# Optimization experiments

Measured on AMD Instinct MI355X. Metric: run time of the kernel, lower is better.

Reference implementation:

```python
import jax, jax.numpy as jnp
import numpy as np

TWO_PI = 2.0 * np.pi
MIN_W = 1e-3  # min bin width (nsf defaults)
MIN_H = 1e-3  # min bin height
MIN_D = 1e-3  # min derivative
NUM_BINS = 32
DERIV_OFFSET = float(np.log(np.e - 1.0))  # so softplus(x+offset)=1 at x=0


def setup_inputs() -> dict:
    key = jax.random.key(0)
    k0, k1, k2, k3 = jax.random.split(key, 4)
    B, N, H, nb, d = 1048576, 64, 256, NUM_BINS, 1
    theta = jax.random.uniform(k0, (B, d), dtype=jnp.float32) * TWO_PI
    x_conditioner = jax.random.normal(k1, (B, N), dtype=jnp.float32)
    W1 = jax.random.normal(k2, (N, H), dtype=jnp.float32) / np.sqrt(N)
    b1 = jnp.zeros((H,), jnp.float32)
    W2 = jax.random.normal(k3, (H, 3 * nb * d), dtype=jnp.float32) / np.sqrt(H)
    b2 = jnp.zeros((3 * nb * d,), jnp.float32)
    eta = jnp.ones((1,), jnp.float32)  # rezero_flag=False -> fixed 1
    return {"theta": theta, "x_conditioner": x_conditioner,
            "W1": W1, "b1": b1, "W2": W2, "b2": b2, "eta": eta}


def _make_knots(unnorm, min_size, left, right):
    # normalized bin sizes -> cumulative knot positions on [left, right]
    nb = unnorm.shape[-1]
    sizes = MIN_W * 0 + min_size + (1.0 - min_size * nb) * jax.nn.softmax(unnorm, axis=-1)
    cum = jnp.cumsum(sizes, axis=-1)
    cum = jnp.concatenate([jnp.zeros_like(cum[..., :1]), cum], axis=-1)
    cum = (right - left) * cum + left
    cum = cum.at[..., 0].set(left)
    cum = cum.at[..., -1].set(right)
    sizes = cum[..., 1:] - cum[..., :-1]
    return cum, sizes


def _circular_rq_spline(inputs, uw, uh, ud, left=0.0, right=TWO_PI):
    # inputs: (B, d); uw/uh/ud: (B, d, nb)
    nb = uw.shape[-1]
    cumwidths, widths = _make_knots(uw, MIN_W, left, right)
    cumheights, heights = _make_knots(uh, MIN_H, left, right)  # circular: bottom=left, top=right
    # circular boundary: derivative at last knot == derivative at first knot
    ud_p = jnp.concatenate([ud, ud[..., :1]], axis=-1)  # (B, d, nb+1)
    derivatives = MIN_D + jax.nn.softplus(ud_p)

    # bin search (searchsorted equivalent)
    bin_idx = jnp.clip(jnp.sum(inputs[..., None] >= cumwidths, axis=-1) - 1, 0, nb - 1)  # (B, d)
    idx = bin_idx[..., None]
    g = lambda t: jnp.take_along_axis(t, idx, axis=-1)[..., 0]

    in_cw = g(cumwidths)
    in_w = g(widths)
    in_ch = g(cumheights)
    in_h = g(heights)
    d_k = g(derivatives)
    d_k1 = jnp.take_along_axis(derivatives, idx + 1, axis=-1)[..., 0]
    delta = in_h / in_w  # bin slope s_k

    th = (inputs - in_cw) / in_w
    th_om = th * (1.0 - th)
    denominator = delta + (d_k1 + d_k - 2.0 * delta) * th_om
    numerator = in_h * (delta * th * th + d_k * th_om)
    outputs = in_ch + numerator / denominator
    deriv_num = delta * delta * (d_k1 * th * th + 2.0 * delta * th_om + d_k * (1.0 - th) ** 2)
    logabsdet = jnp.log(deriv_num) - 2.0 * jnp.log(denominator)
    return outputs, logabsdet


def reference(theta, x_conditioner, W1, b1, W2, b2, eta):
    B, d = theta.shape
    nb = NUM_BINS
    h = jax.nn.relu(x_conditioner @ W1 + b1)
    params = (h @ W2 + b2) * eta
    params = params.reshape(B, d, 3 * nb)
    uw, uh, ud = jnp.split(params, 3, axis=-1)
    ud = ud + DERIV_OFFSET
    theta_out, logabsdet = _circular_rq_spline(theta, uw, uh, ud)
    return theta_out, logabsdet
```

## Files before the change

kernel.cpp:

```cpp
#include <hip/hip_runtime.h>


typedef _Float16 f16x8 __attribute__((ext_vector_type(8)));
typedef float    f32x4 __attribute__((ext_vector_type(4)));

#define TWO_PI_F  6.28318530717958647692f
#define MIN_SZ    1e-3f
#define MIN_D_F   1e-3f
#define DERIV_OFF 0.54132485461291810f

__device__ __forceinline__ float softplus_f(float x) {
    return fmaxf(x, 0.f) + log1pf(__expf(-fabsf(x)));
}

__global__ void flow_prep(const float* __restrict__ W1, const float* __restrict__ W2,
                          _Float16* __restrict__ w1h, _Float16* __restrict__ w1l,
                          _Float16* __restrict__ w2h, _Float16* __restrict__ w2l) {
    int i = blockIdx.x * 256 + threadIdx.x;
    if (i < 16384) {
        int j = i & 7, l = (i >> 3) & 63, kx = (i >> 9) & 1, ht = i >> 10;
        int h = ht * 16 + (l & 15);
        int k = kx * 32 + (l >> 4) * 8 + j;
        float v = W1[k * 256 + h];
        _Float16 hv = (_Float16)v;
        w1h[i] = hv;
        w1l[i] = (_Float16)(v - (float)hv);
    }
    int i2 = i - 16384;
    if (i2 >= 0 && i2 < 24576) {
        int j = i2 & 7, l = (i2 >> 3) & 63, kb = (i2 >> 9) & 7, pt = i2 >> 12;
        int p = pt * 16 + (l & 15);
        int h = (2 * kb + (j >> 2)) * 16 + ((l >> 4) << 2) + (j & 3);
        float v = W2[h * 96 + p];
        _Float16 hv = (_Float16)v;
        w2h[i2] = hv;
        w2l[i2] = (_Float16)(v - (float)hv);
    }
}

__global__ __launch_bounds__(256, 3) void flow_main(
    const float* __restrict__ theta, const float* __restrict__ xc,
    const float* __restrict__ b1g, const float* __restrict__ b2g,
    const float* __restrict__ etag,
    const _Float16* __restrict__ w1h, const _Float16* __restrict__ w1l,
    const _Float16* __restrict__ w2h, const _Float16* __restrict__ w2l,
    float* __restrict__ out, int Btot)
{
    __shared__ __align__(16) float sP[4 * 32 * 97];
    __shared__ float sB1[256];
    __shared__ float sB2[96];

    const int t   = threadIdx.x;
    const int wid = t >> 6;
    const int l   = t & 63;
    const int q   = l >> 4;
    const int lc  = l & 15;
    const long R0w = ((long)blockIdx.x * 4 + wid) * 32;

    if (t < 256) sB1[t] = b1g[t];
    if (t < 96)  sB2[t] = b2g[t];
    __syncthreads();
    const float ev = etag[0];

    float thA = 0.f;
    if (l < 32) thA = theta[R0w + l];

    const f16x8* w1vh = (const f16x8*)w1h;
    const f16x8* w1vl = (const f16x8*)w1l;
    const f16x8* w2vh = (const f16x8*)w2h;
    const f16x8* w2vl = (const f16x8*)w2l;

    f16x8 xh[2][2], xl[2][2];
    #pragma unroll
    for (int mt = 0; mt < 2; ++mt)
        #pragma unroll
        for (int kx = 0; kx < 2; ++kx) {
            const float* xp = xc + (R0w + mt * 16 + lc) * 64 + kx * 32 + q * 8;
            float4 v0 = *(const float4*)xp;
            float4 v1 = *(const float4*)(xp + 4);
            f16x8 hi, lo;
            hi[0] = (_Float16)v0.x; lo[0] = (_Float16)(v0.x - (float)hi[0]);
            hi[1] = (_Float16)v0.y; lo[1] = (_Float16)(v0.y - (float)hi[1]);
            hi[2] = (_Float16)v0.z; lo[2] = (_Float16)(v0.z - (float)hi[2]);
            hi[3] = (_Float16)v0.w; lo[3] = (_Float16)(v0.w - (float)hi[3]);
            hi[4] = (_Float16)v1.x; lo[4] = (_Float16)(v1.x - (float)hi[4]);
            hi[5] = (_Float16)v1.y; lo[5] = (_Float16)(v1.y - (float)hi[5]);
            hi[6] = (_Float16)v1.z; lo[6] = (_Float16)(v1.z - (float)hi[6]);
            hi[7] = (_Float16)v1.w; lo[7] = (_Float16)(v1.w - (float)hi[7]);
            xh[mt][kx] = hi;
            xl[mt][kx] = lo;
        }

    f32x4 acc2[6][2] = {};
    #pragma unroll 2
    for (int kb = 0; kb < 8; ++kb) {
        f32x4 a1[2][2] = {};
        #pragma unroll
        for (int i = 0; i < 2; ++i) {
            const int ht = 2 * kb + i;
            #pragma unroll
            for (int kx = 0; kx < 2; ++kx) {
                f16x8 wh = w1vh[(ht * 2 + kx) * 64 + l];
                f16x8 wl = w1vl[(ht * 2 + kx) * 64 + l];
                #pragma unroll
                for (int mt = 0; mt < 2; ++mt) {
                    a1[i][mt] = __builtin_amdgcn_mfma_f32_16x16x32_f16(wl, xh[mt][kx], a1[i][mt], 0, 0, 0);
                    a1[i][mt] = __builtin_amdgcn_mfma_f32_16x16x32_f16(wh, xl[mt][kx], a1[i][mt], 0, 0, 0);
                    a1[i][mt] = __builtin_amdgcn_mfma_f32_16x16x32_f16(wh, xh[mt][kx], a1[i][mt], 0, 0, 0);
                }
            }
        }
        f16x8 bh[2], bl[2];
        float4 bb0 = *(const float4*)(sB1 + (2 * kb + 0) * 16 + q * 4);
        float4 bb1 = *(const float4*)(sB1 + (2 * kb + 1) * 16 + q * 4);
        #pragma unroll
        for (int mt = 0; mt < 2; ++mt) {
            f16x8 hi, lo;
            float v;
            v = fmaxf(a1[0][mt][0] + bb0.x, 0.f); hi[0] = (_Float16)v; lo[0] = (_Float16)(v - (float)hi[0]);
            v = fmaxf(a1[0][mt][1] + bb0.y, 0.f); hi[1] = (_Float16)v; lo[1] = (_Float16)(v - (float)hi[1]);
            v = fmaxf(a1[0][mt][2] + bb0.z, 0.f); hi[2] = (_Float16)v; lo[2] = (_Float16)(v - (float)hi[2]);
            v = fmaxf(a1[0][mt][3] + bb0.w, 0.f); hi[3] = (_Float16)v; lo[3] = (_Float16)(v - (float)hi[3]);
            v = fmaxf(a1[1][mt][0] + bb1.x, 0.f); hi[4] = (_Float16)v; lo[4] = (_Float16)(v - (float)hi[4]);
            v = fmaxf(a1[1][mt][1] + bb1.y, 0.f); hi[5] = (_Float16)v; lo[5] = (_Float16)(v - (float)hi[5]);
            v = fmaxf(a1[1][mt][2] + bb1.z, 0.f); hi[6] = (_Float16)v; lo[6] = (_Float16)(v - (float)hi[6]);
            v = fmaxf(a1[1][mt][3] + bb1.w, 0.f); hi[7] = (_Float16)v; lo[7] = (_Float16)(v - (float)hi[7]);
            bh[mt] = hi;
            bl[mt] = lo;
        }
        #pragma unroll
        for (int pt = 0; pt < 6; ++pt) {
            f16x8 wh = w2vh[(pt * 8 + kb) * 64 + l];
            f16x8 wl = w2vl[(pt * 8 + kb) * 64 + l];
            #pragma unroll
            for (int mt = 0; mt < 2; ++mt) {
                acc2[pt][mt] = __builtin_amdgcn_mfma_f32_16x16x32_f16(wl, bh[mt], acc2[pt][mt], 0, 0, 0);
                acc2[pt][mt] = __builtin_amdgcn_mfma_f32_16x16x32_f16(wh, bl[mt], acc2[pt][mt], 0, 0, 0);
                acc2[pt][mt] = __builtin_amdgcn_mfma_f32_16x16x32_f16(wh, bh[mt], acc2[pt][mt], 0, 0, 0);
            }
        }
    }

    float* sPw = sP + wid * (32 * 97);
    #pragma unroll
    for (int pt = 0; pt < 6; ++pt) {
        float4 bb = *(const float4*)(sB2 + pt * 16 + q * 4);
        #pragma unroll
        for (int mtl = 0; mtl < 2; ++mtl) {
            f32x4 v = acc2[pt][mtl];
            float* dst = sPw + (mtl * 16 + lc) * 97 + pt * 16 + q * 4;
            dst[0] = (v[0] + bb.x) * ev;
            dst[1] = (v[1] + bb.y) * ev;
            dst[2] = (v[2] + bb.z) * ev;
            dst[3] = (v[3] + bb.w) * ev;
        }
    }
    {
        int row = l & 31;
        float* rowp = sPw + row * 97 + ((l >> 5) << 5);
        float mx = rowp[0];
        #pragma unroll
        for (int j = 1; j < 32; ++j) mx = fmaxf(mx, rowp[j]);
        float S = 0.f;
        #pragma unroll
        for (int j = 0; j < 32; ++j) {
            float e = __expf(rowp[j] - mx);
            rowp[j] = e;
            S += e;
        }
        float scale = (1.0f - 32.0f * MIN_SZ) / S;
        float c = 0.f;
        #pragma unroll
        for (int j = 0; j < 32; ++j) {
            c += rowp[j];
            rowp[j] = TWO_PI_F * fmaf(scale, c, MIN_SZ * (float)(j + 1));
        }
        rowp[31] = TWO_PI_F;
    }
    if (l < 32) {
        const float* row = sPw + l * 97;
        long gr = R0w + l;
        float th_in = thA;
        int bin = 0;
        #pragma unroll
        for (int j = 0; j < 32; ++j) bin += (th_in >= row[j]) ? 1 : 0;
        bin = min(bin, 31);

        float cwk1 = row[bin];
        float cwk0 = (bin == 0) ? 0.f : row[bin - 1];
        float chk1 = row[32 + bin];
        float chk0 = (bin == 0) ? 0.f : row[32 + bin - 1];
        float in_w = cwk1 - cwk0;
        float in_h = chk1 - chk0;
        float d_k  = MIN_D_F + softplus_f(row[64 + bin] + DERIV_OFF);
        float d_k1 = MIN_D_F + softplus_f(row[64 + ((bin + 1) & 31)] + DERIV_OFF);

        float s   = in_h / in_w;
        float tt  = (th_in - cwk0) / in_w;
        float tom = tt * (1.f - tt);
        float denom = s + (d_k1 + d_k - 2.f * s) * tom;
        float numer = in_h * (s * tt * tt + d_k * tom);
        float outv  = chk0 + numer / denom;
        float omt   = 1.f - tt;
        float dnum  = s * s * (d_k1 * tt * tt + 2.f * s * tom + d_k * omt * omt);
        float lad   = __logf(dnum) - 2.f * __logf(denom);

        out[gr]               = outv;
        out[(long)Btot + gr]  = lad;
    }
}

extern "C" void kernel_launch(void* const* d_in, const int* in_sizes, int n_in,
                              void* d_out, int out_size, void* d_ws, size_t ws_size,
                              hipStream_t stream) {
    const float* theta = (const float*)d_in[0];
    const float* xcond = (const float*)d_in[1];
    const float* W1    = (const float*)d_in[2];
    const float* b1    = (const float*)d_in[3];
    const float* W2    = (const float*)d_in[4];
    const float* b2    = (const float*)d_in[5];
    const float* eta   = (const float*)d_in[6];
    int Btot = in_sizes[0];

    _Float16* w1h = (_Float16*)d_ws;
    _Float16* w1l = w1h + 16384;
    _Float16* w2h = w1l + 16384;
    _Float16* w2l = w2h + 24576;

    flow_prep<<<160, 256, 0, stream>>>(W1, W2, w1h, w1l, w2h, w2l);
    flow_main<<<Btot / 128, 256, 0, stream>>>(theta, xcond, b1, b2, eta,
                                              w1h, w1l, w2h, w2l,
                                              (float*)d_out, Btot);
}
```

Baseline: 556.7 us.

## Halve LDS staging by processing spline tail in two 16-row rounds

The epilogue now stages only 16 rows of spline parameters per wave in LDS and processes the two M-tiles in sequence. This halves shared memory per block and raises the launch-bounds occupancy target from 3 to 4 blocks per CU. The softmax/cumsum work is split so each lane handles 16 entries, with the two halves combined through cross-lane shuffles, which uses all 64 lanes instead of 32 rows per pass. In exchange, the tail runs two serial rounds, and the tighter register budget for 4 blocks may cause spills.

```diff
diff --git a/kernel.cpp b/kernel.cpp
--- a/kernel.cpp
+++ b/kernel.cpp
@@ -38,7 +38,7 @@
     }
 }
 
-__global__ __launch_bounds__(256, 3) void flow_main(
+__global__ __launch_bounds__(256, 4) void flow_main(
     const float* __restrict__ theta, const float* __restrict__ xc,
     const float* __restrict__ b1g, const float* __restrict__ b2g,
     const float* __restrict__ etag,
@@ -46,7 +46,7 @@
     const _Float16* __restrict__ w2h, const _Float16* __restrict__ w2l,
     float* __restrict__ out, int Btot)
 {
-    __shared__ __align__(16) float sP[4 * 32 * 97];
+    __shared__ __align__(16) float sP[4 * 16 * 97];
     __shared__ float sB1[256];
     __shared__ float sB2[96];
 
@@ -62,8 +62,11 @@
     __syncthreads();
     const float ev = etag[0];
 
-    float thA = 0.f;
-    if (l < 32) thA = theta[R0w + l];
+    float th0 = 0.f, th1 = 0.f;
+    if (l < 16) {
+        th0 = theta[R0w + l];
+        th1 = theta[R0w + 16 + l];
+    }
 
     const f16x8* w1vh = (const f16x8*)w1h;
     const f16x8* w1vl = (const f16x8*)w1l;
@@ -141,72 +144,85 @@
         }
     }
 
-    float* sPw = sP + wid * (32 * 97);
+    float* sPw = sP + wid * (16 * 97);
+    const int krow  = l & 15;
+    const int kset  = (l >> 4) & 1;
+    const int khalf = l >> 5;
+
     #pragma unroll
-    for (int pt = 0; pt < 6; ++pt) {
-        float4 bb = *(const float4*)(sB2 + pt * 16 + q * 4);
-        #pragma unroll
-        for (int mtl = 0; mtl < 2; ++mtl) {
-            f32x4 v = acc2[pt][mtl];
-            float* dst = sPw + (mtl * 16 + lc) * 97 + pt * 16 + q * 4;
+    for (int rd = 0; rd < 2; ++rd) {
+        #pragma unroll
+        for (int pt = 0; pt < 6; ++pt) {
+            float4 bb = *(const float4*)(sB2 + pt * 16 + q * 4);
+            f32x4 v = acc2[pt][rd];
+            float* dst = sPw + lc * 97 + pt * 16 + q * 4;
             dst[0] = (v[0] + bb.x) * ev;
             dst[1] = (v[1] + bb.y) * ev;
             dst[2] = (v[2] + bb.z) * ev;
             dst[3] = (v[3] + bb.w) * ev;
         }
-    }
-    {
-        int row = l & 31;
-        float* rowp = sPw + row * 97 + ((l >> 5) << 5);
-        float mx = rowp[0];
-        #pragma unroll
-        for (int j = 1; j < 32; ++j) mx = fmaxf(mx, rowp[j]);
-        float S = 0.f;
-        #pragma unroll
-        for (int j = 0; j < 32; ++j) {
-            float e = __expf(rowp[j] - mx);
-            rowp[j] = e;
-            S += e;
-        }
-        float scale = (1.0f - 32.0f * MIN_SZ) / S;
-        float c = 0.f;
-        #pragma unroll
-        for (int j = 0; j < 32; ++j) {
-            c += rowp[j];
-            rowp[j] = TWO_PI_F * fmaf(scale, c, MIN_SZ * (float)(j + 1));
-        }
-        rowp[31] = TWO_PI_F;
-    }
-    if (l < 32) {
-        const float* row = sPw + l * 97;
-        long gr = R0w + l;
-        float th_in = thA;
-        int bin = 0;
-        #pragma unroll
-        for (int j = 0; j < 32; ++j) bin += (th_in >= row[j]) ? 1 : 0;
-        bin = min(bin, 31);
-
-        float cwk1 = row[bin];
-        float cwk0 = (bin == 0) ? 0.f : row[bin - 1];
-        float chk1 = row[32 + bin];
-        float chk0 = (bin == 0) ? 0.f : row[32 + bin - 1];
-        float in_w = cwk1 - cwk0;
-        float in_h = chk1 - chk0;
-        float d_k  = MIN_D_F + softplus_f(row[64 + bin] + DERIV_OFF);
-        float d_k1 = MIN_D_F + softplus_f(row[64 + ((bin + 1) & 31)] + DERIV_OFF);
-
-        float s   = in_h / in_w;
-        float tt  = (th_in - cwk0) / in_w;
-        float tom = tt * (1.f - tt);
-        float denom = s + (d_k1 + d_k - 2.f * s) * tom;
-        float numer = in_h * (s * tt * tt + d_k * tom);
-        float outv  = chk0 + numer / denom;
-        float omt   = 1.f - tt;
-        float dnum  = s * s * (d_k1 * tt * tt + 2.f * s * tom + d_k * omt * omt);
-        float lad   = __logf(dnum) - 2.f * __logf(denom);
-
-        out[gr]               = outv;
-        out[(long)Btot + gr]  = lad;
+        {
+            float* basep = sPw + krow * 97 + kset * 32 + khalf * 16;
+            float tv[16];
+            #pragma unroll
+            for (int j = 0; j < 16; ++j) tv[j] = basep[j];
+            float mx = tv[0];
+            #pragma unroll
+            for (int j = 1; j < 16; ++j) mx = fmaxf(mx, tv[j]);
+            mx = fmaxf(mx, __shfl_xor(mx, 32));
+            float cl = 0.f;
+            #pragma unroll
+            for (int j = 0; j < 16; ++j) {
+                tv[j] = __expf(tv[j] - mx);
+                cl += tv[j];
+            }
+            float cpart = __shfl_xor(cl, 32);
+            float c = khalf ? cpart : 0.f;
+            #pragma unroll
+            for (int j = 0; j < 16; ++j) {
+                c += tv[j];
+                tv[j] = c;
+            }
+            float Sx = __shfl_xor(c, 32);
+            float S = khalf ? c : Sx;
+            float scale = (1.0f - 32.0f * MIN_SZ) / S;
+            float base_off = MIN_SZ * (float)(khalf * 16 + 1);
+            #pragma unroll
+            for (int j = 0; j < 16; ++j)
+                basep[j] = TWO_PI_F * fmaf(scale, tv[j], base_off + MIN_SZ * (float)j);
+            if (khalf) basep[15] = TWO_PI_F;
+        }
+        if (l < 16) {
+            const float* row = sPw + l * 97;
+            long gr = R0w + rd * 16 + l;
+            float th_in = rd ? th1 : th0;
+            int bin = 0;
+            #pragma unroll
+            for (int j = 0; j < 32; ++j) bin += (th_in >= row[j]) ? 1 : 0;
+            bin = min(bin, 31);
+
+            float cwk1 = row[bin];
+            float cwk0 = (bin == 0) ? 0.f : row[bin - 1];
+            float chk1 = row[32 + bin];
+            float chk0 = (bin == 0) ? 0.f : row[32 + bin - 1];
+            float in_w = cwk1 - cwk0;
+            float in_h = chk1 - chk0;
+            float d_k  = MIN_D_F + softplus_f(row[64 + bin] + DERIV_OFF);
+            float d_k1 = MIN_D_F + softplus_f(row[64 + ((bin + 1) & 31)] + DERIV_OFF);
+
+            float s   = in_h / in_w;
+            float tt  = (th_in - cwk0) / in_w;
+            float tom = tt * (1.f - tt);
+            float denom = s + (d_k1 + d_k - 2.f * s) * tom;
+            float numer = in_h * (s * tt * tt + d_k * tom);
+            float outv  = chk0 + numer / denom;
+            float omt   = 1.f - tt;
+            float dnum  = s * s * (d_k1 * tt * tt + 2.f * s * tom + d_k * omt * omt);
+            float lad   = __logf(dnum) - 2.f * __logf(denom);
+
+            out[gr]               = outv;
+            out[(long)Btot + gr]  = lad;
+        }
     }
 }
 
```

Measured after the change: 850.8 us. 1.53x slower.
